# Optimization experiments

Measured on AMD Instinct MI355X. Metric: run time of the kernel, lower is better.

## Reference

```python
import jax, jax.numpy as jnp
import numpy as np

B, LQ, LD, H, C = 128, 32, 512, 768, 128


def setup_inputs() -> dict:
    key = jax.random.key(0)
    ks = jax.random.split(key, 8)
    return {
        "query_hidden": jax.random.normal(ks[0], (B, LQ, H), dtype=jnp.float32),
        "doc_hidden": jax.random.normal(ks[1], (B, LD, H), dtype=jnp.float32),
        "query_mask": jax.random.randint(ks[2], (B, LQ), 0, 2, dtype=jnp.int32),
        "doc_mask": jax.random.randint(ks[3], (B, LD), 0, 2, dtype=jnp.int32),
        "W_comp": jax.random.normal(ks[4], (H, C), dtype=jnp.float32) * (1.0 / np.sqrt(H)),
        "b_comp": jax.random.normal(ks[5], (C,), dtype=jnp.float32) * 0.02,
        "w_stop": jax.random.normal(ks[6], (C, 1), dtype=jnp.float32) * (1.0 / np.sqrt(C)),
        "b_stop": jnp.ones((1,), dtype=jnp.float32),  # nn.init.constant_(bias, 1)
        "score_merger": jnp.zeros((1,), dtype=jnp.float32),
    }


def reference(query_hidden, doc_hidden, query_mask, doc_mask,
              W_comp, b_comp, w_stop, b_stop, score_merger):
    qm = query_mask.astype(bool)  # [B, LQ]
    dm = doc_mask.astype(bool)    # [B, LD]

    # encode_shared: CLS vec is the UNcompressed hidden state at position 0
    q_cls = query_hidden[:, 0, :]  # [B, H]
    d_cls = doc_hidden[:, 0, :]    # [B, H]

    # compressor (Linear H->C)
    q_vecs = jnp.einsum('blh,hc->blc', query_hidden, W_comp) + b_comp  # [B, LQ, C]
    d_tok = jnp.einsum('blh,hc->blc', doc_hidden, W_comp) + b_comp     # [B, LD, C]

    # encode_query: zero masked query tokens
    q_vecs = q_vecs * qm[..., None]

    # encode_doc: stopword reducer (relu of Linear C->1), then importance + mask
    importance = jax.nn.relu(jnp.einsum('blc,co->blo', d_tok, w_stop) + b_stop)  # [B, LD, 1]
    d_vecs = d_tok * importance * dm[..., None]

    # CLS score: dot product of (uncompressed) CLS vectors
    cls_score = jnp.sum(q_cls * d_cls, axis=-1)  # [B]

    # term score: MaxSim over doc tokens, masked sum over query tokens
    scores = jnp.einsum('bqc,bkc->bqk', q_vecs, d_vecs)      # [B, LQ, LD]
    scores = jnp.where(dm[:, None, :], scores, -1000.0)
    term = jnp.max(scores, axis=-1)                          # [B, LQ]
    term_score = jnp.sum(jnp.where(qm, term, 0.0), axis=-1)  # [B]

    w = jax.nn.sigmoid(score_merger[0])
    cls_score = cls_score * w
    term_score = term_score * (1.0 - w)
    score = cls_score + term_score
    return (score, cls_score, term_score)
```

## Files before the change

kernel.cpp:

```cpp
#include <hip/hip_runtime.h>
#include <hip/hip_bf16.h>

#define Bb 128
#define LQ 32
#define LD 512
#define Hh 768
#define Cc 128

#define DBLOCKS ((Bb * LD) / 64)
#define QBLOCKS ((Bb * LQ) / 64)

typedef short bf16x8 __attribute__((ext_vector_type(8)));
typedef short bf16x4 __attribute__((ext_vector_type(4)));
typedef float f32x4 __attribute__((ext_vector_type(4)));

__device__ __forceinline__ short f2bf(float f) {
  union { float f; unsigned u; } v;
  v.f = f;
  unsigned u = v.u + (0x7FFFu + ((v.u >> 16) & 1u));
  return (short)(u >> 16);
}

__global__ __launch_bounds__(256) void k_wt(const float* __restrict__ W,
                                            short* __restrict__ Wt) {
  int idx = blockIdx.x * 256 + threadIdx.x;
  int h = idx >> 7;
  int c = idx & 127;
  Wt[c * Hh + h] = f2bf(W[idx]);
}

__global__ __launch_bounds__(256, 4) void k_proj_q(
    const float* __restrict__ qh, const short* __restrict__ Wt,
    const float* __restrict__ bcomp, const int* __restrict__ qmask,
    float* __restrict__ qv) {
  constexpr int ASTR = 144;
  constexpr int BSTR = 160;
  constexpr int ASZ = 64 * ASTR;
  constexpr int BSZ = 128 * BSTR;
  __shared__ __align__(16) char sm[ASZ + BSZ];

  const int tid = threadIdx.x;
  const int w = tid >> 6;
  const int lane = tid & 63;
  const int quad = lane >> 4;
  const int lm = lane & 15;

  const long row0b = (long)blockIdx.x * 64;

  const float* gA = qh + (row0b + w * 16 + (lane >> 4)) * (long)Hh + (lane & 15) * 4;
  const short* gB = Wt + (w * 32 + (lane >> 3)) * Hh + (lane & 7) * 8;
  const int aoff = (w * 16 + (lane >> 4)) * ASTR + (lane & 15) * 8;
  const int boff = (w * 32 + (lane >> 3)) * BSTR + (lane & 7) * 16;

  char* bufA = sm;
  char* bufB = sm + ASZ;

  f32x4 acc[8];
#pragma unroll
  for (int j = 0; j < 8; ++j) acc[j] = (f32x4){0.f, 0.f, 0.f, 0.f};

  float4 ar[4];
  bf16x8 br[4];
#pragma unroll
  for (int i = 0; i < 4; ++i) ar[i] = *(const float4*)(gA + i * 4 * Hh);
#pragma unroll
  for (int i = 0; i < 4; ++i) br[i] = *(const bf16x8*)(gB + i * 8 * Hh);

  for (int kk = 0; kk < Hh / 64; ++kk) {
    __syncthreads();
#pragma unroll
    for (int i = 0; i < 4; ++i) {
      bf16x4 p;
      p[0] = f2bf(ar[i].x); p[1] = f2bf(ar[i].y);
      p[2] = f2bf(ar[i].z); p[3] = f2bf(ar[i].w);
      *(bf16x4*)(bufA + aoff + i * 4 * ASTR) = p;
    }
#pragma unroll
    for (int i = 0; i < 4; ++i)
      *(bf16x8*)(bufB + boff + i * 8 * BSTR) = br[i];
    __syncthreads();

    {
      const long go = (kk + 1 < Hh / 64) ? (long)(kk + 1) * 64 : 0;
#pragma unroll
      for (int i = 0; i < 4; ++i) ar[i] = *(const float4*)(gA + i * 4 * Hh + go);
#pragma unroll
      for (int i = 0; i < 4; ++i) br[i] = *(const bf16x8*)(gB + i * 8 * Hh + go);
    }

#pragma unroll
    for (int ks = 0; ks < 2; ++ks) {
      bf16x8 fa = *(const bf16x8*)(bufA + (w * 16 + lm) * ASTR + ks * 64 + quad * 16);
#pragma unroll
      for (int j = 0; j < 8; ++j) {
        bf16x8 fb = *(const bf16x8*)(bufB + (j * 16 + lm) * BSTR + ks * 64 + quad * 16);
        acc[j] = __builtin_amdgcn_mfma_f32_16x16x32_bf16(fa, fb, acc[j], 0, 0, 0);
      }
    }
  }

  const long row0 = row0b + w * 16;
  float bc[8];
#pragma unroll
  for (int j = 0; j < 8; ++j) bc[j] = bcomp[j * 16 + lm];

#pragma unroll
  for (int r = 0; r < 4; ++r) {
    const long row = row0 + quad * 4 + r;
    const float scale = (float)qmask[row];
    float* yr = qv + row * Cc;
#pragma unroll
    for (int j = 0; j < 8; ++j) yr[j * 16 + lm] = (acc[j][r] + bc[j]) * scale;
  }
}

__global__ __launch_bounds__(256, 3) void k_doc_score(
    const float* __restrict__ dh, const short* __restrict__ Wt,
    const float* __restrict__ bcomp, const int* __restrict__ dmask,
    const float* __restrict__ wstop, const float* __restrict__ bstop,
    const float* __restrict__ qv, float* __restrict__ partial) {
  constexpr int ASTR = 144;
  constexpr int BSTR = 160;
  constexpr int ASZ = 64 * ASTR;
  constexpr int BSZ = 128 * BSTR;
  constexpr int DSTR = 132;
  constexpr int DVB = 64 * DSTR * 4;
  __shared__ __align__(16) char smem[DVB + 32 * DSTR * 4 + 256 + 2048];

  char* bufA = smem;
  char* bufB = smem + ASZ;
  float* dvt = (float*)smem;
  float* lqt = (float*)(smem + DVB);
  int* dmsk = (int*)(smem + DVB + 32 * DSTR * 4);
  float* pm = (float*)(smem + DVB + 32 * DSTR * 4 + 256);

  const int tid = threadIdx.x;
  const int w = tid >> 6;
  const int lane = tid & 63;
  const int quad = lane >> 4;
  const int lm = lane & 15;

  const int b = blockIdx.x >> 3;
  const int chunk = blockIdx.x & 7;
  const long row0b = (long)b * LD + chunk * 64;

  {
    const float4* src = (const float4*)(qv + (size_t)b * LQ * Cc);
    for (int i = tid; i < LQ * Cc / 4; i += 256) {
      float4 v = src[i];
      int q = i >> 5;
      int c = (i & 31) << 2;
      *(float4*)&lqt[q * DSTR + c] = v;
    }
  }
  if (tid < 64) dmsk[tid] = dmask[row0b + tid];

  const float* gA = dh + (row0b + w * 16 + (lane >> 4)) * (long)Hh + (lane & 15) * 4;
  const short* gB = Wt + (w * 32 + (lane >> 3)) * Hh + (lane & 7) * 8;
  const int aoff = (w * 16 + (lane >> 4)) * ASTR + (lane & 15) * 8;
  const int boff = (w * 32 + (lane >> 3)) * BSTR + (lane & 7) * 16;

  f32x4 acc[8];
#pragma unroll
  for (int j = 0; j < 8; ++j) acc[j] = (f32x4){0.f, 0.f, 0.f, 0.f};

  float4 ar[4];
  bf16x8 br[4];
#pragma unroll
  for (int i = 0; i < 4; ++i) ar[i] = *(const float4*)(gA + i * 4 * Hh);
#pragma unroll
  for (int i = 0; i < 4; ++i) br[i] = *(const bf16x8*)(gB + i * 8 * Hh);

  for (int kk = 0; kk < Hh / 64; ++kk) {
    __syncthreads();
#pragma unroll
    for (int i = 0; i < 4; ++i) {
      bf16x4 p;
      p[0] = f2bf(ar[i].x); p[1] = f2bf(ar[i].y);
      p[2] = f2bf(ar[i].z); p[3] = f2bf(ar[i].w);
      *(bf16x4*)(bufA + aoff + i * 4 * ASTR) = p;
    }
#pragma unroll
    for (int i = 0; i < 4; ++i)
      *(bf16x8*)(bufB + boff + i * 8 * BSTR) = br[i];
    __syncthreads();

    {
      const long go = (kk + 1 < Hh / 64) ? (long)(kk + 1) * 64 : 0;
#pragma unroll
      for (int i = 0; i < 4; ++i) ar[i] = *(const float4*)(gA + i * 4 * Hh + go);
#pragma unroll
      for (int i = 0; i < 4; ++i) br[i] = *(const bf16x8*)(gB + i * 8 * Hh + go);
    }

#pragma unroll
    for (int ks = 0; ks < 2; ++ks) {
      bf16x8 fa = *(const bf16x8*)(bufA + (w * 16 + lm) * ASTR + ks * 64 + quad * 16);
#pragma unroll
      for (int j = 0; j < 8; ++j) {
        bf16x8 fb = *(const bf16x8*)(bufB + (j * 16 + lm) * BSTR + ks * 64 + quad * 16);
        acc[j] = __builtin_amdgcn_mfma_f32_16x16x32_bf16(fa, fb, acc[j], 0, 0, 0);
      }
    }
  }

  __syncthreads();

  float bc[8], wsv[8];
#pragma unroll
  for (int j = 0; j < 8; ++j) bc[j] = bcomp[j * 16 + lm];
#pragma unroll
  for (int j = 0; j < 8; ++j) wsv[j] = wstop[j * 16 + lm];
  const float bs = bstop[0];

#pragma unroll
  for (int r = 0; r < 4; ++r) {
    const int lrow = w * 16 + quad * 4 + r;
    float v[8];
#pragma unroll
    for (int j = 0; j < 8; ++j) v[j] = acc[j][r] + bc[j];
    float p = 0.f;
#pragma unroll
    for (int j = 0; j < 8; ++j) p += v[j] * wsv[j];
    p += __shfl_xor(p, 1);
    p += __shfl_xor(p, 2);
    p += __shfl_xor(p, 4);
    p += __shfl_xor(p, 8);
    const float imp = fmaxf(p + bs, 0.f);
    const float scale = imp * (float)dmsk[lrow];
#pragma unroll
    for (int j = 0; j < 8; ++j) dvt[lrow * DSTR + j * 16 + lm] = v[j] * scale;
  }
  __syncthreads();

  const int qt = tid & 15;
  const int kt = tid >> 4;
  const int kbase = kt * 4;
  float a[2][4];
#pragma unroll
  for (int qi = 0; qi < 2; ++qi)
#pragma unroll
    for (int ki = 0; ki < 4; ++ki) a[qi][ki] = 0.f;

  for (int c = 0; c < Cc; c += 4) {
    float4 q0 = *(float4*)&lqt[qt * DSTR + c];
    float4 q1 = *(float4*)&lqt[(qt + 16) * DSTR + c];
    float4 d0 = *(float4*)&dvt[(kbase + 0) * DSTR + c];
    float4 d1 = *(float4*)&dvt[(kbase + 1) * DSTR + c];
    float4 d2 = *(float4*)&dvt[(kbase + 2) * DSTR + c];
    float4 d3 = *(float4*)&dvt[(kbase + 3) * DSTR + c];
    a[0][0] += q0.x * d0.x + q0.y * d0.y + q0.z * d0.z + q0.w * d0.w;
    a[0][1] += q0.x * d1.x + q0.y * d1.y + q0.z * d1.z + q0.w * d1.w;
    a[0][2] += q0.x * d2.x + q0.y * d2.y + q0.z * d2.z + q0.w * d2.w;
    a[0][3] += q0.x * d3.x + q0.y * d3.y + q0.z * d3.z + q0.w * d3.w;
    a[1][0] += q1.x * d0.x + q1.y * d0.y + q1.z * d0.z + q1.w * d0.w;
    a[1][1] += q1.x * d1.x + q1.y * d1.y + q1.z * d1.z + q1.w * d1.w;
    a[1][2] += q1.x * d2.x + q1.y * d2.y + q1.z * d2.z + q1.w * d2.w;
    a[1][3] += q1.x * d3.x + q1.y * d3.y + q1.z * d3.z + q1.w * d3.w;
  }
  float m0 = -1000.f, m1 = -1000.f;
#pragma unroll
  for (int ki = 0; ki < 4; ++ki) {
    if (dmsk[kbase + ki]) {
      m0 = fmaxf(m0, a[0][ki]);
      m1 = fmaxf(m1, a[1][ki]);
    }
  }
  pm[qt * 16 + kt] = m0;
  pm[(qt + 16) * 16 + kt] = m1;
  __syncthreads();
  if (tid < LQ) {
    float mx = pm[tid * 16];
#pragma unroll
    for (int t = 1; t < 16; ++t) mx = fmaxf(mx, pm[tid * 16 + t]);
    partial[((size_t)b * LQ + tid) * 8 + chunk] = mx;
  }
}

__global__ __launch_bounds__(256) void k_final(
    const float* __restrict__ qh, const float* __restrict__ dh,
    const int* __restrict__ qmask, const float* __restrict__ partial,
    const float* __restrict__ merger, float* __restrict__ out) {
  const int b = blockIdx.x;
  const int tid = threadIdx.x;
  __shared__ float red[256];
  __shared__ float clss;
  const float* qc = qh + (size_t)b * LQ * Hh;
  const float* dc = dh + (size_t)b * LD * Hh;
  float s = 0.f;
  for (int h = tid; h < Hh; h += 256) s += qc[h] * dc[h];
  red[tid] = s;
  __syncthreads();
  for (int off = 128; off > 0; off >>= 1) {
    if (tid < off) red[tid] += red[tid + off];
    __syncthreads();
  }
  if (tid == 0) clss = red[0];
  __syncthreads();
  float t = 0.f;
  if (tid < LQ) {
    const float* pp = partial + ((size_t)b * LQ + tid) * 8;
    float mx = pp[0];
#pragma unroll
    for (int c = 1; c < 8; ++c) mx = fmaxf(mx, pp[c]);
    if (qmask[b * LQ + tid]) t = mx;
  }
  red[tid] = t;
  __syncthreads();
  for (int off = 128; off > 0; off >>= 1) {
    if (tid < off) red[tid] += red[tid + off];
    __syncthreads();
  }
  if (tid == 0) {
    float w = 1.f / (1.f + expf(-merger[0]));
    float cs = clss * w;
    float ts = red[0] * (1.f - w);
    out[b] = cs + ts;
    out[Bb + b] = cs;
    out[2 * Bb + b] = ts;
  }
}

extern "C" void kernel_launch(void* const* d_in, const int* in_sizes, int n_in,
                              void* d_out, int out_size, void* d_ws, size_t ws_size,
                              hipStream_t stream) {
  const float* qh  = (const float*)d_in[0];
  const float* dh  = (const float*)d_in[1];
  const int*   qm  = (const int*)d_in[2];
  const int*   dm  = (const int*)d_in[3];
  const float* W   = (const float*)d_in[4];
  const float* bc  = (const float*)d_in[5];
  const float* wst = (const float*)d_in[6];
  const float* bst = (const float*)d_in[7];
  const float* mrg = (const float*)d_in[8];
  float* out = (float*)d_out;

  char* ws = (char*)d_ws;
  short* Wt  = (short*)ws;
  float* qv  = (float*)(ws + 196608);
  float* prt = (float*)(ws + 196608 + 2097152);

  k_wt<<<(Hh * Cc) / 256, 256, 0, stream>>>(W, Wt);
  k_proj_q<<<QBLOCKS, 256, 0, stream>>>(qh, Wt, bc, qm, qv);
  k_doc_score<<<DBLOCKS, 256, 0, stream>>>(dh, Wt, bc, dm, wst, bst, qv, prt);
  k_final<<<Bb, 256, 0, stream>>>(qh, dh, qm, prt, mrg, out);
}
```

Before: 331.3 us.

## Fuse query projection into doc scoring kernel, recomputing per doc chunk

Removes the separate query-projection kernel and its global qv round trip. Each doc-scoring block now has two of its four waves also project the 32 query rows for its batch element, reading fp32 query hidden states straight from global into MFMA operand registers. The query projection is recomputed 8 times per batch (once per doc chunk), adding extra MFMA work, global reads and register pressure in exchange for one fewer launch and no intermediate buffer.

Result: faster. 319.5 us (-3.6%).

```diff
diff --git a/kernel.cpp b/kernel.cpp
--- a/kernel.cpp
+++ b/kernel.cpp
@@ -8,7 +8,6 @@
 #define Cc 128
 
 #define DBLOCKS ((Bb * LD) / 64)
-#define QBLOCKS ((Bb * LQ) / 64)
 
 typedef short bf16x8 __attribute__((ext_vector_type(8)));
 typedef short bf16x4 __attribute__((ext_vector_type(4)));
@@ -29,100 +28,15 @@
   Wt[c * Hh + h] = f2bf(W[idx]);
 }
 
-__global__ __launch_bounds__(256, 4) void k_proj_q(
-    const float* __restrict__ qh, const short* __restrict__ Wt,
-    const float* __restrict__ bcomp, const int* __restrict__ qmask,
-    float* __restrict__ qv) {
+__global__ __launch_bounds__(256, 3) void k_fused(
+    const float* __restrict__ dh, const float* __restrict__ qh,
+    const short* __restrict__ Wt, const float* __restrict__ bcomp,
+    const int* __restrict__ qmask, const int* __restrict__ dmask,
+    const float* __restrict__ wstop, const float* __restrict__ bstop,
+    float* __restrict__ partial) {
   constexpr int ASTR = 144;
   constexpr int BSTR = 160;
   constexpr int ASZ = 64 * ASTR;
-  constexpr int BSZ = 128 * BSTR;
-  __shared__ __align__(16) char sm[ASZ + BSZ];
-
-  const int tid = threadIdx.x;
-  const int w = tid >> 6;
-  const int lane = tid & 63;
-  const int quad = lane >> 4;
-  const int lm = lane & 15;
-
-  const long row0b = (long)blockIdx.x * 64;
-
-  const float* gA = qh + (row0b + w * 16 + (lane >> 4)) * (long)Hh + (lane & 15) * 4;
-  const short* gB = Wt + (w * 32 + (lane >> 3)) * Hh + (lane & 7) * 8;
-  const int aoff = (w * 16 + (lane >> 4)) * ASTR + (lane & 15) * 8;
-  const int boff = (w * 32 + (lane >> 3)) * BSTR + (lane & 7) * 16;
-
-  char* bufA = sm;
-  char* bufB = sm + ASZ;
-
-  f32x4 acc[8];
-#pragma unroll
-  for (int j = 0; j < 8; ++j) acc[j] = (f32x4){0.f, 0.f, 0.f, 0.f};
-
-  float4 ar[4];
-  bf16x8 br[4];
-#pragma unroll
-  for (int i = 0; i < 4; ++i) ar[i] = *(const float4*)(gA + i * 4 * Hh);
-#pragma unroll
-  for (int i = 0; i < 4; ++i) br[i] = *(const bf16x8*)(gB + i * 8 * Hh);
-
-  for (int kk = 0; kk < Hh / 64; ++kk) {
-    __syncthreads();
-#pragma unroll
-    for (int i = 0; i < 4; ++i) {
-      bf16x4 p;
-      p[0] = f2bf(ar[i].x); p[1] = f2bf(ar[i].y);
-      p[2] = f2bf(ar[i].z); p[3] = f2bf(ar[i].w);
-      *(bf16x4*)(bufA + aoff + i * 4 * ASTR) = p;
-    }
-#pragma unroll
-    for (int i = 0; i < 4; ++i)
-      *(bf16x8*)(bufB + boff + i * 8 * BSTR) = br[i];
-    __syncthreads();
-
-    {
-      const long go = (kk + 1 < Hh / 64) ? (long)(kk + 1) * 64 : 0;
-#pragma unroll
-      for (int i = 0; i < 4; ++i) ar[i] = *(const float4*)(gA + i * 4 * Hh + go);
-#pragma unroll
-      for (int i = 0; i < 4; ++i) br[i] = *(const bf16x8*)(gB + i * 8 * Hh + go);
-    }
-
-#pragma unroll
-    for (int ks = 0; ks < 2; ++ks) {
-      bf16x8 fa = *(const bf16x8*)(bufA + (w * 16 + lm) * ASTR + ks * 64 + quad * 16);
-#pragma unroll
-      for (int j = 0; j < 8; ++j) {
-        bf16x8 fb = *(const bf16x8*)(bufB + (j * 16 + lm) * BSTR + ks * 64 + quad * 16);
-        acc[j] = __builtin_amdgcn_mfma_f32_16x16x32_bf16(fa, fb, acc[j], 0, 0, 0);
-      }
-    }
-  }
-
-  const long row0 = row0b + w * 16;
-  float bc[8];
-#pragma unroll
-  for (int j = 0; j < 8; ++j) bc[j] = bcomp[j * 16 + lm];
-
-#pragma unroll
-  for (int r = 0; r < 4; ++r) {
-    const long row = row0 + quad * 4 + r;
-    const float scale = (float)qmask[row];
-    float* yr = qv + row * Cc;
-#pragma unroll
-    for (int j = 0; j < 8; ++j) yr[j * 16 + lm] = (acc[j][r] + bc[j]) * scale;
-  }
-}
-
-__global__ __launch_bounds__(256, 3) void k_doc_score(
-    const float* __restrict__ dh, const short* __restrict__ Wt,
-    const float* __restrict__ bcomp, const int* __restrict__ dmask,
-    const float* __restrict__ wstop, const float* __restrict__ bstop,
-    const float* __restrict__ qv, float* __restrict__ partial) {
-  constexpr int ASTR = 144;
-  constexpr int BSTR = 160;
-  constexpr int ASZ = 64 * ASTR;
-  constexpr int BSZ = 128 * BSTR;
   constexpr int DSTR = 132;
   constexpr int DVB = 64 * DSTR * 4;
   __shared__ __align__(16) char smem[DVB + 32 * DSTR * 4 + 256 + 2048];
@@ -139,37 +53,37 @@
   const int lane = tid & 63;
   const int quad = lane >> 4;
   const int lm = lane & 15;
+  const bool isq = (w < 2);
 
   const int b = blockIdx.x >> 3;
   const int chunk = blockIdx.x & 7;
   const long row0b = (long)b * LD + chunk * 64;
 
-  {
-    const float4* src = (const float4*)(qv + (size_t)b * LQ * Cc);
-    for (int i = tid; i < LQ * Cc / 4; i += 256) {
-      float4 v = src[i];
-      int q = i >> 5;
-      int c = (i & 31) << 2;
-      *(float4*)&lqt[q * DSTR + c] = v;
-    }
-  }
   if (tid < 64) dmsk[tid] = dmask[row0b + tid];
 
   const float* gA = dh + (row0b + w * 16 + (lane >> 4)) * (long)Hh + (lane & 15) * 4;
   const short* gB = Wt + (w * 32 + (lane >> 3)) * Hh + (lane & 7) * 8;
+  const float* gQ = qh + ((long)b * LQ + w * 16 + lm) * Hh + quad * 8;
   const int aoff = (w * 16 + (lane >> 4)) * ASTR + (lane & 15) * 8;
   const int boff = (w * 32 + (lane >> 3)) * BSTR + (lane & 7) * 16;
 
-  f32x4 acc[8];
+  f32x4 acc[8], accq[8];
 #pragma unroll
   for (int j = 0; j < 8; ++j) acc[j] = (f32x4){0.f, 0.f, 0.f, 0.f};
-
-  float4 ar[4];
+#pragma unroll
+  for (int j = 0; j < 8; ++j) accq[j] = (f32x4){0.f, 0.f, 0.f, 0.f};
+
+  float4 ar[4], aq[4];
   bf16x8 br[4];
 #pragma unroll
   for (int i = 0; i < 4; ++i) ar[i] = *(const float4*)(gA + i * 4 * Hh);
 #pragma unroll
   for (int i = 0; i < 4; ++i) br[i] = *(const bf16x8*)(gB + i * 8 * Hh);
+  if (isq) {
+#pragma unroll
+    for (int i = 0; i < 4; ++i)
+      aq[i] = *(const float4*)(gQ + (i >> 1) * 32 + (i & 1) * 4);
+  }
 
   for (int kk = 0; kk < Hh / 64; ++kk) {
     __syncthreads();
@@ -185,21 +99,41 @@
       *(bf16x8*)(bufB + boff + i * 8 * BSTR) = br[i];
     __syncthreads();
 
+    bf16x8 fq0, fq1;
+    if (isq) {
+      fq0[0] = f2bf(aq[0].x); fq0[1] = f2bf(aq[0].y);
+      fq0[2] = f2bf(aq[0].z); fq0[3] = f2bf(aq[0].w);
+      fq0[4] = f2bf(aq[1].x); fq0[5] = f2bf(aq[1].y);
+      fq0[6] = f2bf(aq[1].z); fq0[7] = f2bf(aq[1].w);
+      fq1[0] = f2bf(aq[2].x); fq1[1] = f2bf(aq[2].y);
+      fq1[2] = f2bf(aq[2].z); fq1[3] = f2bf(aq[2].w);
+      fq1[4] = f2bf(aq[3].x); fq1[5] = f2bf(aq[3].y);
+      fq1[6] = f2bf(aq[3].z); fq1[7] = f2bf(aq[3].w);
+    }
+
     {
       const long go = (kk + 1 < Hh / 64) ? (long)(kk + 1) * 64 : 0;
 #pragma unroll
       for (int i = 0; i < 4; ++i) ar[i] = *(const float4*)(gA + i * 4 * Hh + go);
 #pragma unroll
       for (int i = 0; i < 4; ++i) br[i] = *(const bf16x8*)(gB + i * 8 * Hh + go);
+      if (isq) {
+#pragma unroll
+        for (int i = 0; i < 4; ++i)
+          aq[i] = *(const float4*)(gQ + go + (i >> 1) * 32 + (i & 1) * 4);
+      }
     }
 
 #pragma unroll
     for (int ks = 0; ks < 2; ++ks) {
       bf16x8 fa = *(const bf16x8*)(bufA + (w * 16 + lm) * ASTR + ks * 64 + quad * 16);
+      const bf16x8 fqk = (ks == 0) ? fq0 : fq1;
 #pragma unroll
       for (int j = 0; j < 8; ++j) {
         bf16x8 fb = *(const bf16x8*)(bufB + (j * 16 + lm) * BSTR + ks * 64 + quad * 16);
         acc[j] = __builtin_amdgcn_mfma_f32_16x16x32_bf16(fa, fb, acc[j], 0, 0, 0);
+        if (isq)
+          accq[j] = __builtin_amdgcn_mfma_f32_16x16x32_bf16(fqk, fb, accq[j], 0, 0, 0);
       }
     }
   }
@@ -230,6 +164,17 @@
     const float scale = imp * (float)dmsk[lrow];
 #pragma unroll
     for (int j = 0; j < 8; ++j) dvt[lrow * DSTR + j * 16 + lm] = v[j] * scale;
+  }
+  if (isq) {
+    const int qrow0 = w * 16 + quad * 4;
+#pragma unroll
+    for (int r = 0; r < 4; ++r) {
+      const int qrow = qrow0 + r;
+      const float scale = (float)qmask[b * LQ + qrow];
+#pragma unroll
+      for (int j = 0; j < 8; ++j)
+        lqt[qrow * DSTR + j * 16 + lm] = (accq[j][r] + bc[j]) * scale;
+    }
   }
   __syncthreads();
 
@@ -337,11 +282,9 @@
 
   char* ws = (char*)d_ws;
   short* Wt  = (short*)ws;
-  float* qv  = (float*)(ws + 196608);
-  float* prt = (float*)(ws + 196608 + 2097152);
+  float* prt = (float*)(ws + 196608);
 
   k_wt<<<(Hh * Cc) / 256, 256, 0, stream>>>(W, Wt);
-  k_proj_q<<<QBLOCKS, 256, 0, stream>>>(qh, Wt, bc, qm, qv);
-  k_doc_score<<<DBLOCKS, 256, 0, stream>>>(dh, Wt, bc, dm, wst, bst, qv, prt);
+  k_fused<<<DBLOCKS, 256, 0, stream>>>(dh, qh, Wt, bc, qm, dm, wst, bst, prt);
   k_final<<<Bb, 256, 0, stream>>>(qh, dh, qm, prt, mrg, out);
 }
```
